# Kernel tuning notes

Measured on AMD Instinct MI355X. Metric: run time of the kernel, lower is better.

Reference implementation:

```python
import jax, jax.numpy as jnp
import numpy as np

B, T, F = 64, 512, 512
F2, F4 = F // 2, F // 4
NUM_MOVES = 4


def setup_inputs() -> dict:
    key = jax.random.key(0)
    ks = jax.random.split(key, 12)
    s = 0.02
    return {
        "action_type_index": jax.random.randint(ks[0], (B, T), 0, 2, dtype=jnp.int32),
        "autoregressive_embedding": jax.random.normal(ks[1], (B, T, F), jnp.float32),
        "moves": jax.random.normal(ks[2], (B, T, NUM_MOVES, F2), jnp.float32),
        # guarantee each slot has at least one legal move (the torch code would NaN/error otherwise)
        "moves_mask": jax.random.bernoulli(ks[3], 0.7, (B, T, NUM_MOVES)).at[..., 0].set(True),
        "Wq1": s * jax.random.normal(ks[4], (F, F2), jnp.float32),
        "bq1": jnp.zeros((F2,), jnp.float32),
        "Wq2": s * jax.random.normal(ks[5], (F2, F4), jnp.float32),
        "bq2": jnp.zeros((F4,), jnp.float32),
        "Wk1": s * jax.random.normal(ks[6], (F2, F2), jnp.float32),
        "bk1": jnp.zeros((F2,), jnp.float32),
        "Wk2": s * jax.random.normal(ks[7], (F2, F4), jnp.float32),
        "bk2": jnp.zeros((F4,), jnp.float32),
        "Wp": s * jax.random.normal(ks[8], (F2, F), jnp.float32),
        "bp": jnp.zeros((F,), jnp.float32),
    }


def _legal_policy(logits, legal):
    # softmax over last axis that respects the legality mask, same ops as torch version
    l_min = logits.min(axis=-1, keepdims=True)
    l = jnp.where(legal, logits, l_min)
    l = l - l.max(axis=-1, keepdims=True)
    l = l * legal
    e = jnp.where(legal, jnp.exp(l), 0.0)
    return e / e.sum(axis=-1, keepdims=True)


def reference(action_type_index, autoregressive_embedding, moves, moves_mask,
              Wq1, bq1, Wq2, bq2, Wk1, bk1, Wk2, bk2, Wp, bp):
    # mask fixup: if the whole mask is empty, make everything legal (torch scalar-bool indexing)
    mask = jnp.where(moves_mask.sum() == 0, jnp.bool_(True), moves_mask)

    q = jax.nn.relu(autoregressive_embedding @ Wq1 + bq1) @ Wq2 + bq2   # [B,T,F4]
    k = jax.nn.relu(moves @ Wk1 + bk1) @ Wk2 + bk2                       # [B,T,4,F4]
    move_logits = jnp.einsum('btf,btmf->btm', q, k)                      # [B,T,4]

    move_policy = _legal_policy(move_logits, mask)                       # [B,T,4]

    # multinomial sample per (B,T) slot (deterministic key for reproducibility)
    samp_logits = jnp.where(move_policy > 0, jnp.log(move_policy), -1e30)
    idx = jax.random.categorical(jax.random.key(42), samp_logits, axis=-1)  # [B,T] int32
    move_index = idx.reshape(B, T, 1)

    # gather sampled move embedding (each slot gathers from its own 4 moves)
    move_embedding = jnp.take_along_axis(moves, idx[:, :, None, None], axis=2)[:, :, 0, :]  # [B,T,F2]
    projected_move_embedding = move_embedding @ Wp + bp                  # [B,T,F]

    valid = (action_type_index == 0)[..., None]                          # [B,T,1]
    ar_out = jnp.where(valid, autoregressive_embedding + projected_move_embedding,
                       autoregressive_embedding)
    return move_logits, move_policy, move_index, ar_out, projected_move_embedding
```

## Files before the change

kernel.cpp:

```cpp
#include <hip/hip_runtime.h>

#define B_   64
#define T_   512
#define F_   512
#define F2_  256
#define F4_  128
#define R_   32768
#define RM_  131072

typedef __attribute__((ext_vector_type(8))) short bf16x8;
typedef __attribute__((ext_vector_type(4))) float f32x4;

__device__ __forceinline__ void split_bf16(float a, unsigned short& h, unsigned short& l)
{
    unsigned x  = __float_as_uint(a);
    unsigned rh = x + 0x7FFFu + ((x >> 16) & 1u);
    unsigned short hs = (unsigned short)(rh >> 16);
    float fh = __uint_as_float((unsigned)hs << 16);
    float r  = a - fh;
    unsigned y  = __float_as_uint(r);
    unsigned rl = y + 0x7FFFu + ((y >> 16) & 1u);
    h = hs;
    l = (unsigned short)(rl >> 16);
}

template<bool TRANS>
__global__ __launch_bounds__(256)
void repack_kernel(const float* __restrict__ src, int N, int kbits,
                   unsigned short* __restrict__ hi, unsigned short* __restrict__ lo)
{
    int idx = blockIdx.x * 256 + threadIdx.x;
    int K = 1 << kbits;
    int k = idx & (K - 1);
    int n = idx >> kbits;
    float v = TRANS ? src[(size_t)k * N + n] : src[idx];
    unsigned short h, l;
    split_bf16(v, h, l);
    hi[idx] = h; lo[idx] = l;
}

#define LDSPAD 40

template<int KDIM, int NDIM, bool RELU, bool PROJ>
__global__ __launch_bounds__(256, 2)
void gemm_bf16s(const float* __restrict__ A,
                const unsigned short* __restrict__ Wh,
                const unsigned short* __restrict__ Wl,
                const float* __restrict__ bias,
                float* __restrict__ C,
                const float* __restrict__ idxf,
                const float* __restrict__ moves,
                const float* __restrict__ xres,
                const int*   __restrict__ atype,
                float* __restrict__ out_ar)
{
    __shared__ unsigned short AhS[128 * LDSPAD];
    __shared__ unsigned short AlS[128 * LDSPAD];
    __shared__ unsigned short WhS[128 * LDSPAD];
    __shared__ unsigned short WlS[128 * LDSPAD];

    const int tid  = threadIdx.x;
    const int lane = tid & 63;
    const int wid  = tid >> 6;
    const int wr   = wid >> 1;
    const int wc   = wid & 1;
    const int row0 = blockIdx.x * 128;
    const int col0 = blockIdx.y * 128;

    const int sr = tid >> 1;
    const int sc = (tid & 1) * 16;
    const float* arow;
    if constexpr (PROJ) {
        const int slot = row0 + sr;
        const int mi = (int)idxf[slot];
        arow = moves + ((size_t)slot * 4 + mi) * KDIM;
    } else {
        arow = A + (size_t)(row0 + sr) * KDIM;
    }
    const int wn = tid & 127;
    const unsigned short* wrow = ((tid >> 7) ? Wl : Wh) + (size_t)(col0 + wn) * KDIM;
    unsigned short* wdst = (tid >> 7) ? WlS : WhS;

    const int fr   = lane & 15;
    const int fkg  = (lane >> 4) * 8;
    const int aoff = (wr * 64 + fr) * LDSPAD + fkg;
    const int woff = (wc * 64 + fr) * LDSPAD + fkg;

    f32x4 acc[4][4];
#pragma unroll
    for (int i = 0; i < 4; i++)
#pragma unroll
        for (int j = 0; j < 4; j++) acc[i][j] = {0.f, 0.f, 0.f, 0.f};

    float4 pa[4];
    uint4  pw[4];
#pragma unroll
    for (int i = 0; i < 4; i++) pa[i] = *(const float4*)&arow[sc + i * 4];
#pragma unroll
    for (int i = 0; i < 4; i++) pw[i] = *(const uint4*)&wrow[i * 8];

    for (int k0 = 0; k0 < KDIM; k0 += 32) {
        {
            unsigned hw[8], lw[8];
#pragma unroll
            for (int i = 0; i < 4; i++) {
                unsigned short h0, l0, h1, l1;
                split_bf16(pa[i].x, h0, l0);
                split_bf16(pa[i].y, h1, l1);
                hw[i * 2 + 0] = (unsigned)h0 | ((unsigned)h1 << 16);
                lw[i * 2 + 0] = (unsigned)l0 | ((unsigned)l1 << 16);
                split_bf16(pa[i].z, h0, l0);
                split_bf16(pa[i].w, h1, l1);
                hw[i * 2 + 1] = (unsigned)h0 | ((unsigned)h1 << 16);
                lw[i * 2 + 1] = (unsigned)l0 | ((unsigned)l1 << 16);
            }
            *(uint4*)&AhS[sr * LDSPAD + sc]     = (uint4){hw[0], hw[1], hw[2], hw[3]};
            *(uint4*)&AhS[sr * LDSPAD + sc + 8] = (uint4){hw[4], hw[5], hw[6], hw[7]};
            *(uint4*)&AlS[sr * LDSPAD + sc]     = (uint4){lw[0], lw[1], lw[2], lw[3]};
            *(uint4*)&AlS[sr * LDSPAD + sc + 8] = (uint4){lw[4], lw[5], lw[6], lw[7]};
#pragma unroll
            for (int i = 0; i < 4; i++)
                *(uint4*)&wdst[wn * LDSPAD + i * 8] = pw[i];
        }
        __syncthreads();

        if (k0 + 32 < KDIM) {
#pragma unroll
            for (int i = 0; i < 4; i++) pa[i] = *(const float4*)&arow[k0 + 32 + sc + i * 4];
#pragma unroll
            for (int i = 0; i < 4; i++) pw[i] = *(const uint4*)&wrow[k0 + 32 + i * 8];
        }

        bf16x8 ah[4], al[4], wh[4], wl[4];
#pragma unroll
        for (int i = 0; i < 4; i++) {
            ah[i] = *(const bf16x8*)&AhS[aoff + i * 16 * LDSPAD];
            al[i] = *(const bf16x8*)&AlS[aoff + i * 16 * LDSPAD];
        }
#pragma unroll
        for (int j = 0; j < 4; j++) {
            wh[j] = *(const bf16x8*)&WhS[woff + j * 16 * LDSPAD];
            wl[j] = *(const bf16x8*)&WlS[woff + j * 16 * LDSPAD];
        }
#pragma unroll
        for (int i = 0; i < 4; i++)
#pragma unroll
            for (int j = 0; j < 4; j++) {
                acc[i][j] = __builtin_amdgcn_mfma_f32_16x16x32_bf16(ah[i], wh[j], acc[i][j], 0, 0, 0);
                acc[i][j] = __builtin_amdgcn_mfma_f32_16x16x32_bf16(ah[i], wl[j], acc[i][j], 0, 0, 0);
                acc[i][j] = __builtin_amdgcn_mfma_f32_16x16x32_bf16(al[i], wh[j], acc[i][j], 0, 0, 0);
            }
        __syncthreads();
    }

#pragma unroll
    for (int j = 0; j < 4; j++) {
        const int col = col0 + wc * 64 + j * 16 + fr;
        const float bv = bias ? bias[col] : 0.f;
#pragma unroll
        for (int i = 0; i < 4; i++) {
            const int rbase = row0 + wr * 64 + i * 16 + (lane >> 4) * 4;
#pragma unroll
            for (int r = 0; r < 4; r++) {
                float v = acc[i][j][r] + bv;
                if constexpr (RELU) v = fmaxf(v, 0.f);
                const size_t off = (size_t)(rbase + r) * NDIM + col;
                C[off] = v;
                if constexpr (PROJ) {
                    float xv = xres[off];
                    out_ar[off] = (atype[rbase + r] == 0) ? xv + v : xv;
                }
            }
        }
    }
}

__device__ __forceinline__ void threefry2x32_k42(unsigned int& x0, unsigned int& x1)
{
    const unsigned int ks0 = 0u;
    const unsigned int ks1 = 42u;
    const unsigned int ks2 = 0x1BD11BDAu ^ 42u;
    x0 += ks0; x1 += ks1;
#define TFR(r) { x0 += x1; x1 = (x1 << (r)) | (x1 >> (32 - (r))); x1 ^= x0; }
    TFR(13) TFR(15) TFR(26) TFR(6)
    x0 += ks1; x1 += ks2 + 1u;
    TFR(17) TFR(29) TFR(16) TFR(24)
    x0 += ks2; x1 += ks0 + 2u;
    TFR(13) TFR(15) TFR(26) TFR(6)
    x0 += ks0; x1 += ks1 + 3u;
    TFR(17) TFR(29) TFR(16) TFR(24)
    x0 += ks1; x1 += ks2 + 4u;
    TFR(13) TFR(15) TFR(26) TFR(6)
    x0 += ks2; x1 += ks0 + 5u;
#undef TFR
}

__global__ __launch_bounds__(256)
void logits_kernel(const float* __restrict__ u, const float* __restrict__ Hk,
                   const float* __restrict__ q, const float* __restrict__ bk2,
                   const int* __restrict__ mask,
                   float* __restrict__ out_logits, float* __restrict__ out_policy,
                   float* __restrict__ out_index, float* __restrict__ gaps,
                   int t0)
{
    const int tl   = blockIdx.x * 256 + threadIdx.x;
    const int t    = t0 + tl;
    const int slot = t >> 2;
    const int m    = t & 3;

    const float4* up = (const float4*)&u[(size_t)slot * F2_];
    const float4* hp = (const float4*)&Hk[(size_t)tl * F2_];
    double dot = 0.0;
#pragma unroll
    for (int i = 0; i < 64; i++) {
        float4 a = up[i], b = hp[i];
        dot += (double)a.x * b.x; dot += (double)a.y * b.y;
        dot += (double)a.z * b.z; dot += (double)a.w * b.w;
    }
    {
        const float4* qp = (const float4*)&q[(size_t)slot * F4_];
        const float4* bp = (const float4*)bk2;
        double qb = 0.0;
#pragma unroll
        for (int i = 0; i < 32; i++) {
            float4 a = qp[i], b = bp[i];
            qb += (double)a.x * b.x; qb += (double)a.y * b.y;
            qb += (double)a.z * b.z; qb += (double)a.w * b.w;
        }
        dot += qb;
    }

    const bool legal = (mask[t] != 0);

    double lmin = fmin(dot, __shfl_xor(dot, 1));
    lmin = fmin(lmin, __shfl_xor(lmin, 2));
    const double lm = legal ? dot : lmin;
    double lmax = fmax(lm, __shfl_xor(lm, 1));
    lmax = fmax(lmax, __shfl_xor(lmax, 2));
    const double e = legal ? exp(lm - lmax) : 0.0;
    double esum = e + __shfl_xor(e, 1);
    esum += __shfl_xor(esum, 2);
    const double policy = e / esum;

    out_logits[t] = (float)dot;
    out_policy[t] = (float)policy;

    const double sl = (policy > 0.0) ? log(policy) : -1e30;

    unsigned int x0 = 0u;
    unsigned int x1 = (unsigned int)t;
    threefry2x32_k42(x0, x1);
    const unsigned int bits = x0 ^ x1;

    const float f  = __uint_as_float(0x3f800000u | (bits >> 9)) - 1.0f;
    const float uf = fmaxf(1.17549435e-38f, f);
    const double g = -log(-log((double)uf));
    const double v = sl + g;

    int    best = m;
    double bv   = v;
    {
        double ov = __shfl_xor(bv, 1); int oi = __shfl_xor(best, 1);
        if (ov > bv || (ov == bv && oi < best)) { bv = ov; best = oi; }
        ov = __shfl_xor(bv, 2); oi = __shfl_xor(best, 2);
        if (ov > bv || (ov == bv && oi < best)) { bv = ov; best = oi; }
    }

    double a1 = fmax(v, __shfl_xor(v, 1));
    double b1 = fmin(v, __shfl_xor(v, 1));
    double a2 = __shfl_xor(a1, 2);
    double b2 = __shfl_xor(b1, 2);
    double top2 = (a1 >= a2) ? fmax(a2, b1) : fmax(a1, b2);
    double top1 = fmax(a1, a2);

    if (m == 0) {
        out_index[slot] = (float)best;
        gaps[slot] = (float)(top1 - top2);
    }
}

#define TAU_ 3e-3f

__global__ __launch_bounds__(256)
void cleanup_kernel(const float* __restrict__ x, const float* __restrict__ moves,
                    const int* __restrict__ mask,
                    const float* __restrict__ Wq1, const float* __restrict__ bq1,
                    const float* __restrict__ Wq2, const float* __restrict__ bq2,
                    const float* __restrict__ Wk1, const float* __restrict__ bk1,
                    const float* __restrict__ Wk2, const float* __restrict__ bk2,
                    const float* __restrict__ gaps, float* __restrict__ out_index)
{
    __shared__ double h1[256];
    __shared__ double qv[128];
    __shared__ double kv[128];
    __shared__ double red[256];
    __shared__ double dotS[4];

    const int j = threadIdx.x;
    for (int s = blockIdx.x; s < R_; s += gridDim.x) {
        if (gaps[s] >= TAU_) continue;

        {
            const float* xr = x + (size_t)s * F_;
            double acc = 0.0;
            for (int c = 0; c < F_; c++) acc += (double)xr[c] * (double)Wq1[(size_t)c * F2_ + j];
            h1[j] = fmax(acc + (double)bq1[j], 0.0);
        }
        __syncthreads();
        if (j < F4_) {
            double acc = 0.0;
            for (int c = 0; c < F2_; c++) acc += h1[c] * (double)Wq2[(size_t)c * F4_ + j];
            qv[j] = acc + (double)bq2[j];
        }
        __syncthreads();

        for (int mv = 0; mv < 4; mv++) {
            const float* mr = moves + ((size_t)s * 4 + mv) * F2_;
            double acc = 0.0;
            for (int c = 0; c < F2_; c++) acc += (double)mr[c] * (double)Wk1[(size_t)c * F2_ + j];
            __syncthreads();
            h1[j] = fmax(acc + (double)bk1[j], 0.0);
            __syncthreads();
            if (j < F4_) {
                double a2 = 0.0;
                for (int c = 0; c < F2_; c++) a2 += h1[c] * (double)Wk2[(size_t)c * F4_ + j];
                kv[j] = a2 + (double)bk2[j];
            }
            __syncthreads();
            red[j] = (j < F4_) ? qv[j] * kv[j] : 0.0;
            __syncthreads();
            for (int st = 128; st > 0; st >>= 1) {
                if (j < st) red[j] += red[j + st];
                __syncthreads();
            }
            if (j == 0) dotS[mv] = red[0];
            __syncthreads();
        }

        if (j == 0) {
            double lmin = dotS[0];
#pragma unroll
            for (int mv = 1; mv < 4; mv++) lmin = fmin(lmin, dotS[mv]);
            double lm[4]; bool lg[4];
            double lmax = -1e300;
#pragma unroll
            for (int mv = 0; mv < 4; mv++) {
                lg[mv] = (mask[(size_t)s * 4 + mv] != 0);
                lm[mv] = lg[mv] ? dotS[mv] : lmin;
                lmax = fmax(lmax, lm[mv]);
            }
            double e[4]; double esum = 0.0;
#pragma unroll
            for (int mv = 0; mv < 4; mv++) {
                e[mv] = lg[mv] ? exp(lm[mv] - lmax) : 0.0;
                esum += e[mv];
            }
            int best = -1; double bv = -1e308;
#pragma unroll
            for (int mv = 0; mv < 4; mv++) {
                double pol = e[mv] / esum;
                double sl = (pol > 0.0) ? log(pol) : -1e30;
                unsigned x0 = 0u, x1 = (unsigned)(s * 4 + mv);
                threefry2x32_k42(x0, x1);
                unsigned bits = x0 ^ x1;
                float fu = __uint_as_float(0x3f800000u | (bits >> 9)) - 1.0f;
                float uf = fmaxf(1.17549435e-38f, fu);
                double g = -log(-log((double)uf));
                double v = sl + g;
                if (v > bv) { bv = v; best = mv; }
            }
            out_index[s] = (float)best;
        }
        __syncthreads();
    }
}

template<int KDIM>
__global__ __launch_bounds__(256, 3)
void mlp2_kernel(const float* __restrict__ A,
                 const float* __restrict__ W1, const float* __restrict__ b1,
                 const float* __restrict__ W2, const float* __restrict__ b2,
                 float* __restrict__ out)
{
    __shared__ float H[32][260];
    __shared__ float As[32][20];
    __shared__ float Bs[4096];

    const int tid  = threadIdx.x;
    const int row0 = blockIdx.x * 32;
    const int tx   = tid & 31;
    const int ty   = tid >> 5;

    float acc[4][8];
#pragma unroll
    for (int i = 0; i < 4; i++)
#pragma unroll
        for (int j = 0; j < 8; j++) acc[i][j] = 0.f;

    for (int k0 = 0; k0 < KDIM; k0 += 16) {
        {
            int r = tid >> 3;
            int c = (tid & 7) * 2;
            float2 v = *(const float2*)&A[(size_t)(row0 + r) * KDIM + k0 + c];
            *(float2*)&As[r][c] = v;
        }
        {
            int kk = tid >> 4;
            int c0 = (tid & 15) * 16;
            const float* src = &W1[(size_t)(k0 + kk) * F2_ + c0];
            float* dst = &Bs[kk * F2_ + c0];
#pragma unroll
            for (int j = 0; j < 4; j++) ((float4*)dst)[j] = ((const float4*)src)[j];
        }
        __syncthreads();
#pragma unroll
        for (int kk = 0; kk < 16; kk += 4) {
            float4 a[4];
#pragma unroll
            for (int i = 0; i < 4; i++) a[i] = *(const float4*)&As[ty * 4 + i][kk];
#pragma unroll
            for (int u = 0; u < 4; u++) {
                float4 w0 = *(const float4*)&Bs[(kk + u) * F2_ + tx * 8];
                float4 w1 = *(const float4*)&Bs[(kk + u) * F2_ + tx * 8 + 4];
#pragma unroll
                for (int i = 0; i < 4; i++) {
                    float av = ((const float*)&a[i])[u];
                    acc[i][0] += av * w0.x; acc[i][1] += av * w0.y;
                    acc[i][2] += av * w0.z; acc[i][3] += av * w0.w;
                    acc[i][4] += av * w1.x; acc[i][5] += av * w1.y;
                    acc[i][6] += av * w1.z; acc[i][7] += av * w1.w;
                }
            }
        }
        __syncthreads();
    }
    {
        float4 b1a = *(const float4*)&b1[tx * 8];
        float4 b1b = *(const float4*)&b1[tx * 8 + 4];
        const float bv[8] = {b1a.x, b1a.y, b1a.z, b1a.w, b1b.x, b1b.y, b1b.z, b1b.w};
#pragma unroll
        for (int i = 0; i < 4; i++) {
            float4 h0, h1;
            h0.x = fmaxf(acc[i][0] + bv[0], 0.f);
            h0.y = fmaxf(acc[i][1] + bv[1], 0.f);
            h0.z = fmaxf(acc[i][2] + bv[2], 0.f);
            h0.w = fmaxf(acc[i][3] + bv[3], 0.f);
            h1.x = fmaxf(acc[i][4] + bv[4], 0.f);
            h1.y = fmaxf(acc[i][5] + bv[5], 0.f);
            h1.z = fmaxf(acc[i][6] + bv[6], 0.f);
            h1.w = fmaxf(acc[i][7] + bv[7], 0.f);
            *(float4*)&H[ty * 4 + i][tx * 8]     = h0;
            *(float4*)&H[ty * 4 + i][tx * 8 + 4] = h1;
        }
    }
    __syncthreads();

    float acc2[4][4];
#pragma unroll
    for (int i = 0; i < 4; i++)
#pragma unroll
        for (int j = 0; j < 4; j++) acc2[i][j] = 0.f;

    for (int k0 = 0; k0 < F2_; k0 += 32) {
        {
            int kk = tid >> 3;
            int c0 = (tid & 7) * 16;
            const float* src = &W2[(size_t)(k0 + kk) * F4_ + c0];
            float* dst = &Bs[kk * F4_ + c0];
#pragma unroll
            for (int j = 0; j < 4; j++) ((float4*)dst)[j] = ((const float4*)src)[j];
        }
        __syncthreads();
#pragma unroll
        for (int kk = 0; kk < 32; kk += 4) {
            float4 h[4];
#pragma unroll
            for (int i = 0; i < 4; i++) h[i] = *(const float4*)&H[ty * 4 + i][k0 + kk];
#pragma unroll
            for (int u = 0; u < 4; u++) {
                float4 w = *(const float4*)&Bs[(kk + u) * F4_ + tx * 4];
#pragma unroll
                for (int i = 0; i < 4; i++) {
                    float hv = ((const float*)&h[i])[u];
                    acc2[i][0] += hv * w.x; acc2[i][1] += hv * w.y;
                    acc2[i][2] += hv * w.z; acc2[i][3] += hv * w.w;
                }
            }
        }
        __syncthreads();
    }
    {
        float4 bb = *(const float4*)&b2[tx * 4];
#pragma unroll
        for (int i = 0; i < 4; i++) {
            float4 o;
            o.x = acc2[i][0] + bb.x;
            o.y = acc2[i][1] + bb.y;
            o.z = acc2[i][2] + bb.z;
            o.w = acc2[i][3] + bb.w;
            *(float4*)&out[(size_t)(row0 + ty * 4 + i) * F4_ + tx * 4] = o;
        }
    }
}

__global__ __launch_bounds__(256)
void logits_sample_kernel(const float* __restrict__ Q, const float* __restrict__ Kv,
                          const int* __restrict__ mask,
                          float* __restrict__ out_logits, float* __restrict__ out_policy,
                          float* __restrict__ out_index)
{
    const int t    = blockIdx.x * 256 + threadIdx.x;
    const int slot = t >> 2;
    const int m    = t & 3;

    const float4* qp = (const float4*)&Q[(size_t)slot * F4_];
    const float4* kp = (const float4*)&Kv[(size_t)t * F4_];
    double dot = 0.0;
#pragma unroll
    for (int i = 0; i < 32; i++) {
        float4 a = qp[i], b = kp[i];
        dot += (double)a.x * b.x; dot += (double)a.y * b.y;
        dot += (double)a.z * b.z; dot += (double)a.w * b.w;
    }

    const bool legal = (mask[t] != 0);

    double lmin = fmin(dot, __shfl_xor(dot, 1));
    lmin = fmin(lmin, __shfl_xor(lmin, 2));
    const double lm = legal ? dot : lmin;
    double lmax = fmax(lm, __shfl_xor(lm, 1));
    lmax = fmax(lmax, __shfl_xor(lmax, 2));
    const double e = legal ? exp(lm - lmax) : 0.0;
    double esum = e + __shfl_xor(e, 1);
    esum += __shfl_xor(esum, 2);
    const double policy = e / esum;

    out_logits[t] = (float)dot;
    out_policy[t] = (float)policy;

    const double sl = (policy > 0.0) ? log(policy) : -1e30;

    unsigned int x0 = 0u;
    unsigned int x1 = (unsigned int)t;
    threefry2x32_k42(x0, x1);
    const unsigned int bits = x0 ^ x1;

    const float f  = __uint_as_float(0x3f800000u | (bits >> 9)) - 1.0f;
    const float uf = fmaxf(1.17549435e-38f, f);
    const double g = -log(-log((double)uf));
    const double v = sl + g;

    int    best = m;
    double bv   = v;
    {
        double ov = __shfl_xor(bv, 1); int oi = __shfl_xor(best, 1);
        if (ov > bv || (ov == bv && oi < best)) { bv = ov; best = oi; }
        ov = __shfl_xor(bv, 2); oi = __shfl_xor(best, 2);
        if (ov > bv || (ov == bv && oi < best)) { bv = ov; best = oi; }
    }
    if (m == 0) out_index[slot] = (float)best;
}

__global__ __launch_bounds__(256, 3)
void proj_kernel(const float* __restrict__ moves, const float* __restrict__ idxf,
                 const float* __restrict__ Wp, const float* __restrict__ bp,
                 const float* __restrict__ x, const int* __restrict__ atype,
                 float* __restrict__ out_ar, float* __restrict__ out_proj)
{
    __shared__ float As[32][260];
    __shared__ float Bs[32 * 128];

    const int tid  = threadIdx.x;
    const int row0 = blockIdx.x * 32;
    const int col0 = blockIdx.y * 128;
    const int tx   = tid & 31;
    const int ty   = tid >> 5;

#pragma unroll
    for (int it = 0; it < 8; it++) {
        int r = (tid >> 6) + it * 4;
        int c = (tid & 63) * 4;
        int slot = row0 + r;
        int mi = (int)idxf[slot];
        float4 v = *(const float4*)&moves[((size_t)slot * 4 + mi) * F2_ + c];
        *(float4*)&As[r][c] = v;
    }
    __syncthreads();

    float acc[4][4];
#pragma unroll
    for (int i = 0; i < 4; i++)
#pragma unroll
        for (int j = 0; j < 4; j++) acc[i][j] = 0.f;

    for (int k0 = 0; k0 < F2_; k0 += 32) {
        {
            int kk = tid >> 3;
            int c0 = (tid & 7) * 16;
            const float* src = &Wp[(size_t)(k0 + kk) * F_ + col0 + c0];
            float* dst = &Bs[kk * 128 + c0];
#pragma unroll
            for (int j = 0; j < 4; j++) ((float4*)dst)[j] = ((const float4*)src)[j];
        }
        __syncthreads();
#pragma unroll
        for (int kk = 0; kk < 32; kk += 4) {
            float4 h[4];
#pragma unroll
            for (int i = 0; i < 4; i++) h[i] = *(const float4*)&As[ty * 4 + i][k0 + kk];
#pragma unroll
            for (int u = 0; u < 4; u++) {
                float4 w = *(const float4*)&Bs[(kk + u) * 128 + tx * 4];
#pragma unroll
                for (int i = 0; i < 4; i++) {
                    float hv = ((const float*)&h[i])[u];
                    acc[i][0] += hv * w.x; acc[i][1] += hv * w.y;
                    acc[i][2] += hv * w.z; acc[i][3] += hv * w.w;
                }
            }
        }
        __syncthreads();
    }

    float4 bb = *(const float4*)&bp[col0 + tx * 4];
#pragma unroll
    for (int i = 0; i < 4; i++) {
        int row = row0 + ty * 4 + i;
        float4 p;
        p.x = acc[i][0] + bb.x;
        p.y = acc[i][1] + bb.y;
        p.z = acc[i][2] + bb.z;
        p.w = acc[i][3] + bb.w;
        size_t off = (size_t)row * F_ + col0 + tx * 4;
        *(float4*)&out_proj[off] = p;
        float4 a = *(const float4*)&x[off];
        bool valid = (atype[row] == 0);
        float4 r4;
        r4.x = valid ? a.x + p.x : a.x;
        r4.y = valid ? a.y + p.y : a.y;
        r4.z = valid ? a.z + p.z : a.z;
        r4.w = valid ? a.w + p.w : a.w;
        *(float4*)&out_ar[off] = r4;
    }
}

extern "C" void kernel_launch(void* const* d_in, const int* in_sizes, int n_in,
                              void* d_out, int out_size, void* d_ws, size_t ws_size,
                              hipStream_t stream)
{
    (void)in_sizes; (void)n_in; (void)out_size;

    const int*   atype = (const int*)d_in[0];
    const float* x     = (const float*)d_in[1];
    const float* moves = (const float*)d_in[2];
    const int*   mask  = (const int*)d_in[3];
    const float* Wq1   = (const float*)d_in[4];
    const float* bq1   = (const float*)d_in[5];
    const float* Wq2   = (const float*)d_in[6];
    const float* bq2   = (const float*)d_in[7];
    const float* Wk1   = (const float*)d_in[8];
    const float* bk1   = (const float*)d_in[9];
    const float* Wk2   = (const float*)d_in[10];
    const float* bk2   = (const float*)d_in[11];
    const float* Wp    = (const float*)d_in[12];
    const float* bp    = (const float*)d_in[13];

    float* out_logits = (float*)d_out;
    float* out_policy = out_logits + RM_;
    float* out_index  = out_policy + RM_;
    float* out_ar     = out_index + R_;
    float* out_proj   = out_ar + (size_t)R_ * F_;

    const size_t WS_NEED = (size_t)786432 * 2 + (size_t)R_ * 4;

    if (d_ws != nullptr && ws_size >= WS_NEED) {
        unsigned short* wq1h = (unsigned short*)d_ws;
        unsigned short* wq1l = wq1h + 131072;
        unsigned short* wq2h = wq1l + 131072;
        unsigned short* wq2l = wq2h + 32768;
        unsigned short* wk1h = wq2l + 32768;
        unsigned short* wk1l = wk1h + 65536;
        unsigned short* wk2h = wk1l + 65536;
        unsigned short* wk2l = wk2h + 32768;
        unsigned short* wph  = wk2l + 32768;
        unsigned short* wpl  = wph + 131072;
        float* gaps = (float*)(wpl + 131072);

        float* Hq = out_ar;
        float* qv = out_ar + 8388608;
        float* uv = out_proj;
        float* Hk = out_ar;

        repack_kernel<true ><<<512, 256, 0, stream>>>(Wq1, F2_, 9, wq1h, wq1l);
        repack_kernel<true ><<<128, 256, 0, stream>>>(Wq2, F4_, 8, wq2h, wq2l);
        repack_kernel<true ><<<256, 256, 0, stream>>>(Wk1, F2_, 8, wk1h, wk1l);
        repack_kernel<false><<<128, 256, 0, stream>>>(Wk2, F4_, 7, wk2h, wk2l);
        repack_kernel<true ><<<512, 256, 0, stream>>>(Wp,  F_,  8, wph,  wpl);

        dim3 g1(R_ / 128, 2);
        gemm_bf16s<512, 256, true,  false><<<g1, 256, 0, stream>>>(
            x, wq1h, wq1l, bq1, Hq, nullptr, nullptr, nullptr, nullptr, nullptr);
        dim3 g2(R_ / 128, 1);
        gemm_bf16s<256, 128, false, false><<<g2, 256, 0, stream>>>(
            Hq, wq2h, wq2l, bq2, qv, nullptr, nullptr, nullptr, nullptr, nullptr);
        dim3 g3(R_ / 128, 2);
        gemm_bf16s<128, 256, false, false><<<g3, 256, 0, stream>>>(
            qv, wk2h, wk2l, nullptr, uv, nullptr, nullptr, nullptr, nullptr, nullptr);

        for (int qi = 0; qi < 4; qi++) {
            const float* mseg = moves + (size_t)qi * 32768 * F2_;
            gemm_bf16s<256, 256, true, false><<<g3, 256, 0, stream>>>(
                mseg, wk1h, wk1l, bk1, Hk, nullptr, nullptr, nullptr, nullptr, nullptr);
            logits_kernel<<<128, 256, 0, stream>>>(
                uv, Hk, qv, bk2, mask, out_logits, out_policy, out_index, gaps, qi * 32768);
        }

        cleanup_kernel<<<2048, 256, 0, stream>>>(
            x, moves, mask, Wq1, bq1, Wq2, bq2, Wk1, bk1, Wk2, bk2, gaps, out_index);

        dim3 gp(R_ / 128, 4);
        gemm_bf16s<256, 512, false, true><<<gp, 256, 0, stream>>>(
            nullptr, wph, wpl, bp, out_proj, out_index, moves, x, atype, out_ar);
    } else {
        float* Q  = out_proj;
        float* Kv = out_ar;

        mlp2_kernel<F_><<<R_ / 32, 256, 0, stream>>>(x, Wq1, bq1, Wq2, bq2, Q);
        mlp2_kernel<F2_><<<RM_ / 32, 256, 0, stream>>>(moves, Wk1, bk1, Wk2, bk2, Kv);
        logits_sample_kernel<<<RM_ / 256, 256, 0, stream>>>(Q, Kv, mask,
                                                            out_logits, out_policy, out_index);
        dim3 pgrid(R_ / 32, 4);
        proj_kernel<<<pgrid, 256, 0, stream>>>(moves, out_index, Wp, bp, x, atype,
                                               out_ar, out_proj);
    }
}
```

Before: 876.6 us.

## Compact near-tie slots into a list and tile fp64 cleanup weights through LDS

A new single-block kernel compacts the slots whose top-two sampling gap falls below the threshold into an index list. A rewritten fp64 recompute kernel then runs only over that list on 128 blocks, instead of 2048 blocks each scanning all 32768 slots. Inside the kernel, weight tiles are staged through shared memory with float4 loads, all four moves are computed at once so Wk1 and Wk2 are shared, and the dot product uses wave shuffles instead of a shared-memory tree reduction. The trade-offs are an extra serial kernel launch, an atomic-based list whose order is not deterministic, and a larger shared-memory footprint.

```diff
diff --git a/kernel.cpp b/kernel.cpp
--- a/kernel.cpp
+++ b/kernel.cpp
@@ -281,63 +281,146 @@
 
 #define TAU_ 3e-3f
 
+__global__ __launch_bounds__(1024)
+void compact_kernel(const float* __restrict__ gaps,
+                    int* __restrict__ cnt, int* __restrict__ list)
+{
+    __shared__ int c;
+    if (threadIdx.x == 0) c = 0;
+    __syncthreads();
+    for (int s = threadIdx.x; s < R_; s += 1024) {
+        if (gaps[s] < TAU_) list[atomicAdd(&c, 1)] = s;
+    }
+    __syncthreads();
+    if (threadIdx.x == 0) *cnt = c;
+}
+
 __global__ __launch_bounds__(256)
-void cleanup_kernel(const float* __restrict__ x, const float* __restrict__ moves,
-                    const int* __restrict__ mask,
-                    const float* __restrict__ Wq1, const float* __restrict__ bq1,
-                    const float* __restrict__ Wq2, const float* __restrict__ bq2,
-                    const float* __restrict__ Wk1, const float* __restrict__ bk1,
-                    const float* __restrict__ Wk2, const float* __restrict__ bk2,
-                    const float* __restrict__ gaps, float* __restrict__ out_index)
-{
-    __shared__ double h1[256];
+void cleanup2_kernel(const float* __restrict__ x, const float* __restrict__ moves,
+                     const int* __restrict__ mask,
+                     const float* __restrict__ Wq1, const float* __restrict__ bq1,
+                     const float* __restrict__ Wq2, const float* __restrict__ bq2,
+                     const float* __restrict__ Wk1, const float* __restrict__ bk1,
+                     const float* __restrict__ Wk2, const float* __restrict__ bk2,
+                     const int* __restrict__ cnt, const int* __restrict__ list,
+                     float* __restrict__ out_index)
+{
+    __shared__ float  xs[512];
+    __shared__ float  mvs[1024];
+    __shared__ float  ws[16 * 256];
+    __shared__ double h1q[256];
+    __shared__ double h1k[4][256];
     __shared__ double qv[128];
-    __shared__ double kv[128];
-    __shared__ double red[256];
-    __shared__ double dotS[4];
+    __shared__ double kv[4][128];
+    __shared__ double wred[8];
 
     const int j = threadIdx.x;
-    for (int s = blockIdx.x; s < R_; s += gridDim.x) {
-        if (gaps[s] >= TAU_) continue;
+    const int n = *cnt;
+
+    for (int ii = blockIdx.x; ii < n; ii += gridDim.x) {
+        const int s = list[ii];
+        __syncthreads();
+
+        *(float2*)&xs[j * 2] = *(const float2*)&x[(size_t)s * F_ + j * 2];
+        ((float4*)mvs)[j] = ((const float4*)&moves[(size_t)s * 4 * F2_])[j];
+
+        double a0 = 0.0, a1 = 0.0;
+        for (int c0 = 0; c0 < 512; c0 += 16) {
+            __syncthreads();
+#pragma unroll
+            for (int u = 0; u < 4; u++) {
+                int idx = u * 256 + j;
+                int r = idx >> 6, c4 = (idx & 63) * 4;
+                *(float4*)&ws[r * 256 + c4] = *(const float4*)&Wq1[(size_t)(c0 + r) * F2_ + c4];
+            }
+            __syncthreads();
+#pragma unroll
+            for (int c = 0; c < 16; c += 2) {
+                a0 += (double)xs[c0 + c]     * (double)ws[c * 256 + j];
+                a1 += (double)xs[c0 + c + 1] * (double)ws[(c + 1) * 256 + j];
+            }
+        }
+        h1q[j] = fmax(a0 + a1 + (double)bq1[j], 0.0);
+
+        double q0 = 0.0, q1 = 0.0;
+        for (int c0 = 0; c0 < 256; c0 += 32) {
+            __syncthreads();
+#pragma unroll
+            for (int u = 0; u < 4; u++) {
+                int idx = u * 256 + j;
+                int r = idx >> 5, c4 = (idx & 31) * 4;
+                *(float4*)&ws[r * 128 + c4] = *(const float4*)&Wq2[(size_t)(c0 + r) * F4_ + c4];
+            }
+            __syncthreads();
+            if (j < 128) {
+#pragma unroll
+                for (int c = 0; c < 32; c += 2) {
+                    q0 += h1q[c0 + c]     * (double)ws[c * 128 + j];
+                    q1 += h1q[c0 + c + 1] * (double)ws[(c + 1) * 128 + j];
+                }
+            }
+        }
+        if (j < 128) qv[j] = q0 + q1 + (double)bq2[j];
+
+        double k0 = 0.0, k1 = 0.0, k2 = 0.0, k3 = 0.0;
+        for (int c0 = 0; c0 < 256; c0 += 16) {
+            __syncthreads();
+#pragma unroll
+            for (int u = 0; u < 4; u++) {
+                int idx = u * 256 + j;
+                int r = idx >> 6, c4 = (idx & 63) * 4;
+                *(float4*)&ws[r * 256 + c4] = *(const float4*)&Wk1[(size_t)(c0 + r) * F2_ + c4];
+            }
+            __syncthreads();
+#pragma unroll
+            for (int c = 0; c < 16; c++) {
+                double w = (double)ws[c * 256 + j];
+                k0 += (double)mvs[0 * 256 + c0 + c] * w;
+                k1 += (double)mvs[1 * 256 + c0 + c] * w;
+                k2 += (double)mvs[2 * 256 + c0 + c] * w;
+                k3 += (double)mvs[3 * 256 + c0 + c] * w;
+            }
+        }
+        h1k[0][j] = fmax(k0 + (double)bk1[j], 0.0);
+        h1k[1][j] = fmax(k1 + (double)bk1[j], 0.0);
+        h1k[2][j] = fmax(k2 + (double)bk1[j], 0.0);
+        h1k[3][j] = fmax(k3 + (double)bk1[j], 0.0);
+
+        const int jj = j & 127, mh = j >> 7;
+        double v0 = 0.0, v1 = 0.0;
+        for (int c0 = 0; c0 < 256; c0 += 32) {
+            __syncthreads();
+#pragma unroll
+            for (int u = 0; u < 4; u++) {
+                int idx = u * 256 + j;
+                int r = idx >> 5, c4 = (idx & 31) * 4;
+                *(float4*)&ws[r * 128 + c4] = *(const float4*)&Wk2[(size_t)(c0 + r) * F4_ + c4];
+            }
+            __syncthreads();
+#pragma unroll
+            for (int c = 0; c < 32; c++) {
+                double w = (double)ws[c * 128 + jj];
+                v0 += h1k[mh][c0 + c]     * w;
+                v1 += h1k[mh + 2][c0 + c] * w;
+            }
+        }
+        kv[mh][jj]     = v0 + (double)bk2[jj];
+        kv[mh + 2][jj] = v1 + (double)bk2[jj];
+        __syncthreads();
 
         {
-            const float* xr = x + (size_t)s * F_;
-            double acc = 0.0;
-            for (int c = 0; c < F_; c++) acc += (double)xr[c] * (double)Wq1[(size_t)c * F2_ + j];
-            h1[j] = fmax(acc + (double)bq1[j], 0.0);
-        }
-        __syncthreads();
-        if (j < F4_) {
-            double acc = 0.0;
-            for (int c = 0; c < F2_; c++) acc += h1[c] * (double)Wq2[(size_t)c * F4_ + j];
-            qv[j] = acc + (double)bq2[j];
-        }
-        __syncthreads();
-
-        for (int mv = 0; mv < 4; mv++) {
-            const float* mr = moves + ((size_t)s * 4 + mv) * F2_;
-            double acc = 0.0;
-            for (int c = 0; c < F2_; c++) acc += (double)mr[c] * (double)Wk1[(size_t)c * F2_ + j];
-            __syncthreads();
-            h1[j] = fmax(acc + (double)bk1[j], 0.0);
-            __syncthreads();
-            if (j < F4_) {
-                double a2 = 0.0;
-                for (int c = 0; c < F2_; c++) a2 += h1[c] * (double)Wk2[(size_t)c * F4_ + j];
-                kv[j] = a2 + (double)bk2[j];
-            }
-            __syncthreads();
-            red[j] = (j < F4_) ? qv[j] * kv[j] : 0.0;
-            __syncthreads();
-            for (int st = 128; st > 0; st >>= 1) {
-                if (j < st) red[j] += red[j + st];
-                __syncthreads();
-            }
-            if (j == 0) dotS[mv] = red[0];
-            __syncthreads();
-        }
+            const int w = j >> 6, l = j & 63;
+            double d = qv[l] * kv[w][l] + qv[l + 64] * kv[w][l + 64];
+#pragma unroll
+            for (int o = 32; o; o >>= 1) d += __shfl_xor(d, o);
+            if (l == 0) wred[w] = d;
+        }
+        __syncthreads();
 
         if (j == 0) {
+            double dotS[4];
+#pragma unroll
+            for (int mv = 0; mv < 4; mv++) dotS[mv] = wred[mv];
             double lmin = dotS[0];
 #pragma unroll
             for (int mv = 1; mv < 4; mv++) lmin = fmin(lmin, dotS[mv]);
@@ -360,9 +443,9 @@
             for (int mv = 0; mv < 4; mv++) {
                 double pol = e[mv] / esum;
                 double sl = (pol > 0.0) ? log(pol) : -1e30;
-                unsigned x0 = 0u, x1 = (unsigned)(s * 4 + mv);
-                threefry2x32_k42(x0, x1);
-                unsigned bits = x0 ^ x1;
+                unsigned xx0 = 0u, xx1 = (unsigned)(s * 4 + mv);
+                threefry2x32_k42(xx0, xx1);
+                unsigned bits = xx0 ^ xx1;
                 float fu = __uint_as_float(0x3f800000u | (bits >> 9)) - 1.0f;
                 float uf = fmaxf(1.17549435e-38f, fu);
                 double g = -log(-log((double)uf));
@@ -371,7 +454,6 @@
             }
             out_index[s] = (float)best;
         }
-        __syncthreads();
     }
 }
 
@@ -690,6 +772,8 @@
         float* qv = out_ar + 8388608;
         float* uv = out_proj;
         float* Hk = out_ar;
+        int* cl_cnt  = (int*)(out_ar + 12582912);
+        int* cl_list = cl_cnt + 16;
 
         repack_kernel<true ><<<512, 256, 0, stream>>>(Wq1, F2_, 9, wq1h, wq1l);
         repack_kernel<true ><<<128, 256, 0, stream>>>(Wq2, F4_, 8, wq2h, wq2l);
@@ -715,8 +799,10 @@
                 uv, Hk, qv, bk2, mask, out_logits, out_policy, out_index, gaps, qi * 32768);
         }
 
-        cleanup_kernel<<<2048, 256, 0, stream>>>(
-            x, moves, mask, Wq1, bq1, Wq2, bq2, Wk1, bk1, Wk2, bk2, gaps, out_index);
+        compact_kernel<<<1, 1024, 0, stream>>>(gaps, cl_cnt, cl_list);
+        cleanup2_kernel<<<128, 256, 0, stream>>>(
+            x, moves, mask, Wq1, bq1, Wq2, bq2, Wk1, bk1, Wk2, bk2,
+            cl_cnt, cl_list, out_index);
 
         dim3 gp(R_ / 128, 4);
         gemm_bf16s<256, 512, false, true><<<gp, 256, 0, stream>>>(
```

New measurement: 822.4 us. -6.2%, faster.
